# Kernel tuning notes

Measured on AMD Instinct MI355X. Metric: run time of the kernel, lower is better.

## Reference

```python
import jax, jax.numpy as jnp
import numpy as np

EPS_RMS = 1.1920929e-07  # torch F.rms_norm default eps = finfo(float32).eps
N_EMBD = 64
N_QKV = 256


def _silu(t):
    return t * jax.nn.sigmoid(t)


def _rms_norm(t):
    return t * jax.lax.rsqrt(jnp.mean(t * t, axis=-1, keepdims=True) + EPS_RMS)


def _w_norm(w, n):
    target_std = n ** (-0.5)
    return w * (target_std / (jnp.std(w, ddof=1) + 1e-08))


def setup_inputs() -> dict:
    key = jax.random.key(0)
    ks = jax.random.split(key, 7)
    B, T = 8, 8192
    x = jax.random.normal(ks[0], (B, T, N_EMBD), dtype=jnp.float32)
    y = jax.random.normal(ks[1], (B, T, N_QKV), dtype=jnp.float32)
    # CastedLinear init: uniform(-s, s), s = sqrt(3)/sqrt(in_features)
    def lin(k, out_f, in_f):
        s = (3.0 ** 0.5) * in_f ** (-0.5)
        return jax.random.uniform(k, (out_f, in_f), jnp.float32, -s, s)
    w_qkv = lin(ks[2], 3 * N_QKV, N_EMBD)          # [768, 64]
    w_swiglu = lin(ks[3], 2 * N_EMBD, N_QKV)       # [128, 256]
    w_out = lin(ks[4], N_EMBD, N_EMBD)             # [64, 64]
    out_w = lin(ks[5], N_EMBD, N_EMBD)             # self.out weight [64, 64]
    tao = lin(ks[6], 3, 1)                          # [3, 1]
    return {"x": x, "y": y, "w_qkv": w_qkv, "w_swiglu": w_swiglu,
            "w_out": w_out, "out_w": out_w, "tao": tao}


def reference(x, y, w_qkv, w_swiglu, w_out, out_w, tao):
    B = x.shape[0]
    # SwiGLU branch: F.linear(y, w_swiglu) -> [B,T,2*n_embd], chunk
    uv = jnp.einsum('btq,eq->bte', y, w_swiglu)
    u, v = jnp.split(uv, 2, axis=-1)                 # each [B,T,64]
    y_out = x + jnp.einsum('btd,ed->bte', u * _silu(v), w_out)

    # gates
    g = jnp.clip(jnp.abs(tao), 1e-08, 1.0)           # [3,1]
    alpha, beta, gamma = g[0], g[1], g[2]

    # Hebbian outer-product memory: mean_b(u^T v) * n_embd^-0.5, rms-normed
    ao = jnp.einsum('btd,bte->de', u, v) / B * (N_EMBD ** (-0.5))  # [64,64]
    ao = _rms_norm(ao)

    # update w_qkv
    n1 = _silu(w_qkv @ ao)                            # [768,64]
    w_qkv_new = _w_norm(w_qkv + n1 @ out_w.T, N_EMBD) * alpha

    # update w_swiglu: view(64, 512).T @ ao
    n2 = _silu(w_swiglu.reshape(N_EMBD, 2 * N_QKV).T @ ao)  # [512,64]
    n2 = n2 @ out_w.T                                  # [512,64]
    w_swiglu_new = w_swiglu + n2.T.reshape(2 * N_EMBD, N_QKV)
    w_swiglu_new = _w_norm(w_swiglu_new, N_QKV) * beta

    # update w_out
    n3 = _silu(w_out @ ao)                             # [64,64]
    w_out_new = _w_norm(w_out + n3 @ out_w.T, N_QKV) * gamma

    return (y_out, w_qkv_new, w_swiglu_new, w_out_new)
```

## Files before the change

### kernel.cpp

```cpp
#include <hip/hip_runtime.h>
#include <cstdint>

typedef short short8 __attribute__((ext_vector_type(8)));
typedef short short4_t __attribute__((ext_vector_type(4)));
typedef float floatx4 __attribute__((ext_vector_type(4)));

#define MFMA_BF16 __builtin_amdgcn_mfma_f32_16x16x32_bf16

__device__ __forceinline__ short f2bf(float f) {
  union { float f; unsigned u; } a; a.f = f;
  unsigned r = a.u + 0x7FFFu + ((a.u >> 16) & 1u);
  return (short)(r >> 16);
}
__device__ __forceinline__ float bf2f(short s) {
  union { unsigned u; float f; } a;
  a.u = ((unsigned)(unsigned short)s) << 16;
  return a.f;
}
__device__ __forceinline__ float silu_f(float v) {
  return v / (1.0f + __expf(-v));
}

#define QDIM 256
#define DEMB 64
#define TILE_T 32
#define ITERS 2
#define NBLK1 1024
#define YSTR 264
#define TSTR 40
#define HSTR 72

#define OFF_QKV 4194304
#define OFF_SW  4243456
#define OFF_WO  4276224

#define AO_COPIES 16
#define WS_SUMS   65536
#define WS_AOT    65544
#define WS_W1P    67592
#define WS_W2P    83976

__global__ __launch_bounds__(256) void k0_pack(
    const float* __restrict__ w_sw, const float* __restrict__ w_out,
    short* __restrict__ W1P, short* __restrict__ W2P,
    float* __restrict__ ws_base)
{
  int t = blockIdx.x * 256 + threadIdx.x;
  if (t < 16386) {
    float4 z = {0.f, 0.f, 0.f, 0.f};
    ((float4*)ws_base)[t] = z;
  }
  if (t < 4096) {
    int lane = t & 63, kt = (t >> 6) & 7, ntw = t >> 9;
    int row = (ntw >> 1) * 32 + (ntw & 1) * 16 + (lane & 15);
    int col = kt * 32 + (lane >> 4) * 8;
    const float* p = w_sw + row * QDIM + col;
    short8 f;
#pragma unroll
    for (int j = 0; j < 8; ++j) f[j] = f2bf(p[j]);
    ((short8*)W1P)[t] = f;
  } else if (t < 4608) {
    int u = t - 4096;
    int lane = u & 63, ktw = u >> 6;
    int row = (ktw >> 1) * 16 + (lane & 15);
    int col = (ktw & 1) * 32 + (lane >> 4) * 8;
    const float* p = w_out + row * DEMB + col;
    short8 f;
#pragma unroll
    for (int j = 0; j < 8; ++j) f[j] = f2bf(p[j]);
    ((short8*)W2P)[u] = f;
  }
}

__global__ __launch_bounds__(256, 3) void k1_main(
    const float* __restrict__ x, const float* __restrict__ y,
    const short* __restrict__ W1P, const short* __restrict__ W2P,
    float* __restrict__ y_out, float* __restrict__ ao_copies)
{
  __shared__ __align__(16) short Ylds[2][TILE_T * YSTR];
  __shared__ __align__(16) short UVT[128 * TSTR];
  __shared__ __align__(16) short Hlds[TILE_T * HSTR];

  const int tid  = threadIdx.x;
  const int lane = tid & 63;
  const int wave = tid >> 6;
  const int l15  = lane & 15;
  const int quad = lane >> 4;
  const floatx4 fzero = {0.f, 0.f, 0.f, 0.f};
  const int tok0 = blockIdx.x * (TILE_T * ITERS);

  const short8* W1v = (const short8*)W1P;
  const short8* W2v = (const short8*)W2P;
  short8 b1[2][8];
#pragma unroll
  for (int nt = 0; nt < 2; ++nt)
#pragma unroll
    for (int kt = 0; kt < 8; ++kt)
      b1[nt][kt] = W1v[((wave * 2 + nt) * 8 + kt) * 64 + lane];
  short8 b2[2];
#pragma unroll
  for (int kt = 0; kt < 2; ++kt)
    b2[kt] = W2v[(wave * 2 + kt) * 64 + lane];

  floatx4 ao_acc[4];
#pragma unroll
  for (int i = 0; i < 4; ++i) ao_acc[i] = fzero;

  float4 yreg[8];
  {
    const float4* src = (const float4*)(y + (size_t)tok0 * QDIM);
#pragma unroll
    for (int rep = 0; rep < 8; ++rep) yreg[rep] = src[tid + rep * 256];
#pragma unroll
    for (int rep = 0; rep < 8; ++rep) {
      int i = tid + rep * 256;
      int tok = i >> 6;
      int col = (i & 63) * 4;
      float4 f = yreg[rep];
      short4_t p4 = { f2bf(f.x), f2bf(f.y), f2bf(f.z), f2bf(f.w) };
      *(short4_t*)&Ylds[0][tok * YSTR + col] = p4;
    }
  }
  float xreg[8];
  __syncthreads();

  for (int it = 0; it < ITERS; ++it) {
    const int cur = it & 1;

    if (it + 1 < ITERS) {
      const float4* src = (const float4*)(y + (size_t)(tok0 + (it + 1) * TILE_T) * QDIM);
#pragma unroll
      for (int rep = 0; rep < 8; ++rep) yreg[rep] = src[tid + rep * 256];
    }
    if (it > 0) {
      const int tb = tok0 + (it - 1) * TILE_T;
#pragma unroll
      for (int mt = 0; mt < 2; ++mt) {
        floatx4 acc2 = fzero;
#pragma unroll
        for (int kt = 0; kt < 2; ++kt) {
          short8 a2 = *(const short8*)&Hlds[(mt * 16 + l15) * HSTR + kt * 32 + quad * 8];
          acc2 = MFMA_BF16(a2, b2[kt], acc2, 0, 0, 0);
        }
        int e = wave * 16 + l15;
#pragma unroll
        for (int r = 0; r < 4; ++r) {
          size_t idx = (size_t)(tb + mt * 16 + quad * 4 + r) * DEMB + e;
          y_out[idx] = xreg[mt * 4 + r] + acc2[r];
        }
      }
    }
    floatx4 acc[2][2];
#pragma unroll
    for (int a = 0; a < 2; ++a)
#pragma unroll
      for (int b = 0; b < 2; ++b) acc[a][b] = fzero;
#pragma unroll
    for (int kt = 0; kt < 8; ++kt) {
      short8 a0 = *(const short8*)&Ylds[cur][(l15)      * YSTR + kt * 32 + quad * 8];
      short8 a1 = *(const short8*)&Ylds[cur][(16 + l15) * YSTR + kt * 32 + quad * 8];
      acc[0][0] = MFMA_BF16(a0, b1[0][kt], acc[0][0], 0, 0, 0);
      acc[0][1] = MFMA_BF16(a0, b1[1][kt], acc[0][1], 0, 0, 0);
      acc[1][0] = MFMA_BF16(a1, b1[0][kt], acc[1][0], 0, 0, 0);
      acc[1][1] = MFMA_BF16(a1, b1[1][kt], acc[1][1], 0, 0, 0);
    }
#pragma unroll
    for (int mt = 0; mt < 2; ++mt)
#pragma unroll
      for (int nt = 0; nt < 2; ++nt) {
        short4_t p4;
#pragma unroll
        for (int r = 0; r < 4; ++r) p4[r] = f2bf(acc[mt][nt][r]);
        int c  = wave * 32 + nt * 16 + l15;
        int t0 = mt * 16 + quad * 4;
        *(short4_t*)&UVT[c * TSTR + t0] = p4;
      }
    __syncthreads();

    {
      const float* xb = x + (size_t)(tok0 + it * TILE_T) * DEMB + wave * 16 + l15;
#pragma unroll
      for (int mt = 0; mt < 2; ++mt)
#pragma unroll
        for (int r = 0; r < 4; ++r)
          xreg[mt * 4 + r] = xb[(mt * 16 + quad * 4 + r) * DEMB];
    }
    {
      int d  = tid & 63;
      int t0 = (tid >> 6) * 8;
      short8 u8 = *(const short8*)&UVT[d * TSTR + t0];
      short8 v8 = *(const short8*)&UVT[(64 + d) * TSTR + t0];
#pragma unroll
      for (int j = 0; j < 8; ++j) {
        float h = bf2f(u8[j]) * silu_f(bf2f(v8[j]));
        Hlds[(t0 + j) * HSTR + d] = f2bf(h);
      }
    }
    {
      short8 a3 = *(const short8*)&UVT[(wave * 16 + l15) * TSTR + quad * 8];
#pragma unroll
      for (int et = 0; et < 4; ++et) {
        short8 b3 = *(const short8*)&UVT[(64 + et * 16 + l15) * TSTR + quad * 8];
        ao_acc[et] = MFMA_BF16(a3, b3, ao_acc[et], 0, 0, 0);
      }
    }
    if (it + 1 < ITERS) {
#pragma unroll
      for (int rep = 0; rep < 8; ++rep) {
        int i = tid + rep * 256;
        int tok = i >> 6;
        int col = (i & 63) * 4;
        float4 f = yreg[rep];
        short4_t p4 = { f2bf(f.x), f2bf(f.y), f2bf(f.z), f2bf(f.w) };
        *(short4_t*)&Ylds[1 - cur][tok * YSTR + col] = p4;
      }
    }
    __syncthreads();
  }

  {
    const int tb = tok0 + (ITERS - 1) * TILE_T;
#pragma unroll
    for (int mt = 0; mt < 2; ++mt) {
      floatx4 acc2 = fzero;
#pragma unroll
      for (int kt = 0; kt < 2; ++kt) {
        short8 a2 = *(const short8*)&Hlds[(mt * 16 + l15) * HSTR + kt * 32 + quad * 8];
        acc2 = MFMA_BF16(a2, b2[kt], acc2, 0, 0, 0);
      }
      int e = wave * 16 + l15;
#pragma unroll
      for (int r = 0; r < 4; ++r) {
        size_t idx = (size_t)(tb + mt * 16 + quad * 4 + r) * DEMB + e;
        y_out[idx] = xreg[mt * 4 + r] + acc2[r];
      }
    }
  }

  float* dst = ao_copies + (blockIdx.x & (AO_COPIES - 1)) * 4096;
#pragma unroll
  for (int et = 0; et < 4; ++et)
#pragma unroll
    for (int r = 0; r < 4; ++r) {
      int d = wave * 16 + quad * 4 + r;
      int e = et * 16 + l15;
      atomicAdd(&dst[d * 64 + e], ao_acc[et][r]);
    }
}

__global__ __launch_bounds__(256) void k2_finalize(
    const float* __restrict__ ao_copies, unsigned short* __restrict__ aoT)
{
  __shared__ float aoFT[64 * 65];
  __shared__ float ssPart[256];
  __shared__ float scRow[64];
  const int tid = threadIdx.x;

#pragma unroll
  for (int k = 0; k < 16; ++k) {
    int idx = k * 256 + tid;
    float v = 0.f;
#pragma unroll
    for (int c = 0; c < AO_COPIES; ++c) v += ao_copies[c * 4096 + idx];
    v *= (1.0f / 64.0f);
    int d = idx >> 6, e = idx & 63;
    aoFT[e * 65 + d] = v;
  }
  __syncthreads();
  {
    int d = tid >> 2, q = tid & 3;
    float ssp = 0.f;
#pragma unroll
    for (int e2 = 0; e2 < 16; ++e2) {
      float v = aoFT[(q * 16 + e2) * 65 + d];
      ssp += v * v;
    }
    ssPart[tid] = ssp;
  }
  __syncthreads();
  if (tid < 64) {
    float ss = ssPart[tid * 4] + ssPart[tid * 4 + 1] +
               ssPart[tid * 4 + 2] + ssPart[tid * 4 + 3];
    scRow[tid] = rsqrtf(ss * (1.0f / 64.0f) + 1.1920929e-07f);
  }
  __syncthreads();
#pragma unroll
  for (int k = 0; k < 16; ++k) {
    int j = k * 256 + tid;
    int e = j >> 6, d = j & 63;
    aoT[j] = (unsigned short)f2bf(aoFT[e * 65 + d] * scRow[d]);
  }
}

__global__ __launch_bounds__(64) void k3_updates(
    const float* __restrict__ w_qkv, const float* __restrict__ w_sw,
    const float* __restrict__ w_out, const float* __restrict__ out_w,
    const unsigned short* __restrict__ aoT, float* __restrict__ out,
    float* __restrict__ sums)
{
  __shared__ __align__(16) short Nlds[16 * 72];
  const int lane = threadIdx.x;
  const int l15  = lane & 15;
  const int quad = lane >> 4;
  const int rid  = blockIdx.x;
  const floatx4 fzero = {0.f, 0.f, 0.f, 0.f};
  const short8* aoTv = (const short8*)aoT;

  short8 bf[2][4];
#pragma unroll
  for (int kt = 0; kt < 2; ++kt)
#pragma unroll
    for (int nt = 0; nt < 4; ++nt)
      bf[kt][nt] = aoTv[(nt * 16 + l15) * 8 + kt * 4 + quad];

  short8 af[2];
  if (rid < 48) {
    const float* wr = w_qkv + (size_t)(rid * 16 + l15) * 64;
#pragma unroll
    for (int kt = 0; kt < 2; ++kt) {
      const float* p = wr + kt * 32 + quad * 8;
      short8 f;
#pragma unroll
      for (int j = 0; j < 8; ++j) f[j] = f2bf(p[j]);
      af[kt] = f;
    }
  } else if (rid < 80) {
    int p0 = (rid - 48) * 16;
#pragma unroll
    for (int kt = 0; kt < 2; ++kt) {
      short8 f;
#pragma unroll
      for (int j = 0; j < 8; ++j) {
        int a = kt * 32 + quad * 8 + j;
        f[j] = f2bf(w_sw[a * 512 + p0 + l15]);
      }
      af[kt] = f;
    }
  } else {
    const float* wr = w_out + (size_t)((rid - 80) * 16 + l15) * 64;
#pragma unroll
    for (int kt = 0; kt < 2; ++kt) {
      const float* p = wr + kt * 32 + quad * 8;
      short8 f;
#pragma unroll
      for (int j = 0; j < 8; ++j) f[j] = f2bf(p[j]);
      af[kt] = f;
    }
  }

  floatx4 acc[4];
#pragma unroll
  for (int nt = 0; nt < 4; ++nt) acc[nt] = fzero;
#pragma unroll
  for (int kt = 0; kt < 2; ++kt)
#pragma unroll
    for (int nt = 0; nt < 4; ++nt)
      acc[nt] = MFMA_BF16(af[kt], bf[kt][nt], acc[nt], 0, 0, 0);
#pragma unroll
  for (int nt = 0; nt < 4; ++nt)
#pragma unroll
    for (int r = 0; r < 4; ++r)
      Nlds[(quad * 4 + r) * 72 + nt * 16 + l15] = f2bf(silu_f(acc[nt][r]));
  __syncthreads();

  float s1 = 0.f, s2 = 0.f;
  int matrix;

  if (rid < 48 || rid >= 80) {
    matrix = (rid < 48) ? 0 : 2;
    short8 a2[2];
#pragma unroll
    for (int kt = 0; kt < 2; ++kt)
      a2[kt] = *(const short8*)&Nlds[l15 * 72 + kt * 32 + quad * 8];
    short8 b2[2][4];
#pragma unroll
    for (int nt = 0; nt < 4; ++nt) {
      const float* wr = out_w + (size_t)(nt * 16 + l15) * 64;
#pragma unroll
      for (int kt = 0; kt < 2; ++kt) {
        const float* p = wr + kt * 32 + quad * 8;
        short8 f;
#pragma unroll
        for (int j = 0; j < 8; ++j) f[j] = f2bf(p[j]);
        b2[kt][nt] = f;
      }
    }
    floatx4 acc2[4];
#pragma unroll
    for (int nt = 0; nt < 4; ++nt) acc2[nt] = fzero;
#pragma unroll
    for (int kt = 0; kt < 2; ++kt)
#pragma unroll
      for (int nt = 0; nt < 4; ++nt)
        acc2[nt] = MFMA_BF16(a2[kt], b2[kt][nt], acc2[nt], 0, 0, 0);

    const float* Wsrc = (rid < 48) ? w_qkv : w_out;
    int base_row = (rid < 48) ? rid * 16 : (rid - 80) * 16;
    int off      = (rid < 48) ? OFF_QKV : OFF_WO;
#pragma unroll
    for (int nt = 0; nt < 4; ++nt)
#pragma unroll
      for (int r = 0; r < 4; ++r) {
        int row = base_row + quad * 4 + r;
        int col = nt * 16 + l15;
        float val = Wsrc[row * 64 + col] + acc2[nt][r];
        out[off + row * 64 + col] = val;
        s1 += val; s2 += val * val;
      }
  } else {
    matrix = 1;
    int p0 = (rid - 48) * 16;
    short8 b2[2];
#pragma unroll
    for (int kt = 0; kt < 2; ++kt)
      b2[kt] = *(const short8*)&Nlds[l15 * 72 + kt * 32 + quad * 8];
    short8 a2[4][2];
#pragma unroll
    for (int mt = 0; mt < 4; ++mt) {
      const float* wr = out_w + (size_t)(mt * 16 + l15) * 64;
#pragma unroll
      for (int kt = 0; kt < 2; ++kt) {
        const float* p = wr + kt * 32 + quad * 8;
        short8 f;
#pragma unroll
        for (int j = 0; j < 8; ++j) f[j] = f2bf(p[j]);
        a2[mt][kt] = f;
      }
    }
    floatx4 acc2[4];
#pragma unroll
    for (int mt = 0; mt < 4; ++mt) acc2[mt] = fzero;
#pragma unroll
    for (int mt = 0; mt < 4; ++mt)
#pragma unroll
      for (int kt = 0; kt < 2; ++kt)
        acc2[mt] = MFMA_BF16(a2[mt][kt], b2[kt], acc2[mt], 0, 0, 0);
#pragma unroll
    for (int mt = 0; mt < 4; ++mt)
#pragma unroll
      for (int r = 0; r < 4; ++r) {
        int a = mt * 16 + quad * 4 + r;
        int p = p0 + l15;
        int idx = a * 512 + p;
        float val = w_sw[idx] + acc2[mt][r];
        out[OFF_SW + idx] = val;
        s1 += val; s2 += val * val;
      }
  }

#pragma unroll
  for (int off = 32; off > 0; off >>= 1) {
    s1 += __shfl_down(s1, off);
    s2 += __shfl_down(s2, off);
  }
  if (lane == 0) {
    atomicAdd(&sums[matrix * 2],     s1);
    atomicAdd(&sums[matrix * 2 + 1], s2);
  }
}

__global__ __launch_bounds__(256) void k4_scale(
    float* __restrict__ out, const float* __restrict__ sums,
    const float* __restrict__ tao)
{
  int i = blockIdx.x * 256 + threadIdx.x;
  int matrix, idx; float N, tstd;
  if (i < 49152)      { matrix = 0; idx = OFF_QKV + i;           N = 49152.f; tstd = 0.125f;  }
  else if (i < 81920) { matrix = 1; idx = OFF_SW + (i - 49152);  N = 32768.f; tstd = 0.0625f; }
  else                { matrix = 2; idx = OFF_WO + (i - 81920);  N = 4096.f;  tstd = 0.0625f; }
  float sum = sums[matrix * 2], sumsq = sums[matrix * 2 + 1];
  float mean = sum / N;
  float var  = (sumsq - N * mean * mean) / (N - 1.f);
  float sd   = sqrtf(fmaxf(var, 0.f));
  float g    = fminf(fmaxf(fabsf(tao[matrix]), 1e-8f), 1.0f);
  out[idx] *= g * tstd / (sd + 1e-8f);
}

extern "C" void kernel_launch(void* const* d_in, const int* in_sizes, int n_in,
                              void* d_out, int out_size, void* d_ws, size_t ws_size,
                              hipStream_t stream) {
  const float* x     = (const float*)d_in[0];
  const float* y     = (const float*)d_in[1];
  const float* w_qkv = (const float*)d_in[2];
  const float* w_sw  = (const float*)d_in[3];
  const float* w_out = (const float*)d_in[4];
  const float* out_w = (const float*)d_in[5];
  const float* tao   = (const float*)d_in[6];
  float* out = (float*)d_out;
  float* ws  = (float*)d_ws;

  float* ao_copies    = ws;
  float* sums         = ws + WS_SUMS;
  unsigned short* aoT = (unsigned short*)(ws + WS_AOT);
  short* W1P          = (short*)(ws + WS_W1P);
  short* W2P          = (short*)(ws + WS_W2P);

  k0_pack<<<dim3(65), dim3(256), 0, stream>>>(w_sw, w_out, W1P, W2P, ws);
  k1_main<<<dim3(NBLK1), dim3(256), 0, stream>>>(x, y, W1P, W2P, out, ao_copies);
  k2_finalize<<<dim3(1), dim3(256), 0, stream>>>(ao_copies, aoT);
  k3_updates<<<dim3(84), dim3(64), 0, stream>>>(w_qkv, w_sw, w_out, out_w,
                                                aoT, out, sums);
  k4_scale<<<dim3(336), dim3(256), 0, stream>>>(out, sums, tao);
}
```

Before: 143.1 us.

## Fuse ao finalize into update kernel; use nontemporal loads/stores in main kernel

Merges the single-block ao finalize kernel into the weight-update kernel. Each of 21 four-wave blocks now redundantly reduces the ao copies, RMS-normalises them and keeps the transposed bf16 ao in LDS, which removes one launch and a global round trip. The main kernel also switches the streaming x/y loads and y_out stores to nontemporal builtins, and silu uses a fast divide. The cost is that every update block repeats the 16-copy reduction.

```diff
diff --git a/kernel.cpp b/kernel.cpp
--- a/kernel.cpp
+++ b/kernel.cpp
@@ -4,6 +4,7 @@
 typedef short short8 __attribute__((ext_vector_type(8)));
 typedef short short4_t __attribute__((ext_vector_type(4)));
 typedef float floatx4 __attribute__((ext_vector_type(4)));
+typedef float floatv4 __attribute__((ext_vector_type(4)));
 
 #define MFMA_BF16 __builtin_amdgcn_mfma_f32_16x16x32_bf16
 
@@ -18,7 +19,7 @@
   return a.f;
 }
 __device__ __forceinline__ float silu_f(float v) {
-  return v / (1.0f + __expf(-v));
+  return v * __fdividef(1.0f, 1.0f + __expf(-v));
 }
 
 #define QDIM 256
@@ -36,9 +37,8 @@
 
 #define AO_COPIES 16
 #define WS_SUMS   65536
-#define WS_AOT    65544
-#define WS_W1P    67592
-#define WS_W2P    83976
+#define WS_W1P    65544
+#define WS_W2P    81928
 
 __global__ __launch_bounds__(256) void k0_pack(
     const float* __restrict__ w_sw, const float* __restrict__ w_out,
@@ -106,17 +106,18 @@
 #pragma unroll
   for (int i = 0; i < 4; ++i) ao_acc[i] = fzero;
 
-  float4 yreg[8];
+  floatv4 yreg[8];
   {
-    const float4* src = (const float4*)(y + (size_t)tok0 * QDIM);
-#pragma unroll
-    for (int rep = 0; rep < 8; ++rep) yreg[rep] = src[tid + rep * 256];
+    const floatv4* src = (const floatv4*)(y + (size_t)tok0 * QDIM);
+#pragma unroll
+    for (int rep = 0; rep < 8; ++rep)
+      yreg[rep] = __builtin_nontemporal_load(&src[tid + rep * 256]);
 #pragma unroll
     for (int rep = 0; rep < 8; ++rep) {
       int i = tid + rep * 256;
       int tok = i >> 6;
       int col = (i & 63) * 4;
-      float4 f = yreg[rep];
+      floatv4 f = yreg[rep];
       short4_t p4 = { f2bf(f.x), f2bf(f.y), f2bf(f.z), f2bf(f.w) };
       *(short4_t*)&Ylds[0][tok * YSTR + col] = p4;
     }
@@ -128,9 +129,10 @@
     const int cur = it & 1;
 
     if (it + 1 < ITERS) {
-      const float4* src = (const float4*)(y + (size_t)(tok0 + (it + 1) * TILE_T) * QDIM);
-#pragma unroll
-      for (int rep = 0; rep < 8; ++rep) yreg[rep] = src[tid + rep * 256];
+      const floatv4* src = (const floatv4*)(y + (size_t)(tok0 + (it + 1) * TILE_T) * QDIM);
+#pragma unroll
+      for (int rep = 0; rep < 8; ++rep)
+        yreg[rep] = __builtin_nontemporal_load(&src[tid + rep * 256]);
     }
     if (it > 0) {
       const int tb = tok0 + (it - 1) * TILE_T;
@@ -146,7 +148,7 @@
 #pragma unroll
         for (int r = 0; r < 4; ++r) {
           size_t idx = (size_t)(tb + mt * 16 + quad * 4 + r) * DEMB + e;
-          y_out[idx] = xreg[mt * 4 + r] + acc2[r];
+          __builtin_nontemporal_store(xreg[mt * 4 + r] + acc2[r], &y_out[idx]);
         }
       }
     }
@@ -183,7 +185,7 @@
       for (int mt = 0; mt < 2; ++mt)
 #pragma unroll
         for (int r = 0; r < 4; ++r)
-          xreg[mt * 4 + r] = xb[(mt * 16 + quad * 4 + r) * DEMB];
+          xreg[mt * 4 + r] = __builtin_nontemporal_load(&xb[(mt * 16 + quad * 4 + r) * DEMB]);
     }
     {
       int d  = tid & 63;
@@ -210,7 +212,7 @@
         int i = tid + rep * 256;
         int tok = i >> 6;
         int col = (i & 63) * 4;
-        float4 f = yreg[rep];
+        floatv4 f = yreg[rep];
         short4_t p4 = { f2bf(f.x), f2bf(f.y), f2bf(f.z), f2bf(f.w) };
         *(short4_t*)&Ylds[1 - cur][tok * YSTR + col] = p4;
       }
@@ -232,7 +234,7 @@
 #pragma unroll
       for (int r = 0; r < 4; ++r) {
         size_t idx = (size_t)(tb + mt * 16 + quad * 4 + r) * DEMB + e;
-        y_out[idx] = xreg[mt * 4 + r] + acc2[r];
+        __builtin_nontemporal_store(xreg[mt * 4 + r] + acc2[r], &y_out[idx]);
       }
     }
   }
@@ -248,13 +250,24 @@
     }
 }
 
-__global__ __launch_bounds__(256) void k2_finalize(
-    const float* __restrict__ ao_copies, unsigned short* __restrict__ aoT)
+__global__ __launch_bounds__(256) void k3_updates(
+    const float* __restrict__ w_qkv, const float* __restrict__ w_sw,
+    const float* __restrict__ w_out, const float* __restrict__ out_w,
+    const float* __restrict__ ao_copies, float* __restrict__ out,
+    float* __restrict__ sums)
 {
   __shared__ float aoFT[64 * 65];
   __shared__ float ssPart[256];
   __shared__ float scRow[64];
-  const int tid = threadIdx.x;
+  __shared__ __align__(16) short aoT[64 * 72];
+  __shared__ __align__(16) short Nlds[4][16 * 72];
+
+  const int tid  = threadIdx.x;
+  const int lane = tid & 63;
+  const int wave = tid >> 6;
+  const int l15  = lane & 15;
+  const int quad = lane >> 4;
+  const floatx4 fzero = {0.f, 0.f, 0.f, 0.f};
 
 #pragma unroll
   for (int k = 0; k < 16; ++k) {
@@ -288,30 +301,18 @@
   for (int k = 0; k < 16; ++k) {
     int j = k * 256 + tid;
     int e = j >> 6, d = j & 63;
-    aoT[j] = (unsigned short)f2bf(aoFT[e * 65 + d] * scRow[d]);
-  }
-}
-
-__global__ __launch_bounds__(64) void k3_updates(
-    const float* __restrict__ w_qkv, const float* __restrict__ w_sw,
-    const float* __restrict__ w_out, const float* __restrict__ out_w,
-    const unsigned short* __restrict__ aoT, float* __restrict__ out,
-    float* __restrict__ sums)
-{
-  __shared__ __align__(16) short Nlds[16 * 72];
-  const int lane = threadIdx.x;
-  const int l15  = lane & 15;
-  const int quad = lane >> 4;
-  const int rid  = blockIdx.x;
-  const floatx4 fzero = {0.f, 0.f, 0.f, 0.f};
-  const short8* aoTv = (const short8*)aoT;
+    aoT[e * 72 + d] = f2bf(aoFT[e * 65 + d] * scRow[d]);
+  }
+  __syncthreads();
+
+  const int rid = blockIdx.x * 4 + wave;
 
   short8 bf[2][4];
 #pragma unroll
   for (int kt = 0; kt < 2; ++kt)
 #pragma unroll
     for (int nt = 0; nt < 4; ++nt)
-      bf[kt][nt] = aoTv[(nt * 16 + l15) * 8 + kt * 4 + quad];
+      bf[kt][nt] = *(const short8*)&aoT[(nt * 16 + l15) * 72 + kt * 32 + quad * 8];
 
   short8 af[2];
   if (rid < 48) {
@@ -360,7 +361,7 @@
   for (int nt = 0; nt < 4; ++nt)
 #pragma unroll
     for (int r = 0; r < 4; ++r)
-      Nlds[(quad * 4 + r) * 72 + nt * 16 + l15] = f2bf(silu_f(acc[nt][r]));
+      Nlds[wave][(quad * 4 + r) * 72 + nt * 16 + l15] = f2bf(silu_f(acc[nt][r]));
   __syncthreads();
 
   float s1 = 0.f, s2 = 0.f;
@@ -371,7 +372,7 @@
     short8 a2[2];
 #pragma unroll
     for (int kt = 0; kt < 2; ++kt)
-      a2[kt] = *(const short8*)&Nlds[l15 * 72 + kt * 32 + quad * 8];
+      a2[kt] = *(const short8*)&Nlds[wave][l15 * 72 + kt * 32 + quad * 8];
     short8 b2[2][4];
 #pragma unroll
     for (int nt = 0; nt < 4; ++nt) {
@@ -413,7 +414,7 @@
     short8 b2[2];
 #pragma unroll
     for (int kt = 0; kt < 2; ++kt)
-      b2[kt] = *(const short8*)&Nlds[l15 * 72 + kt * 32 + quad * 8];
+      b2[kt] = *(const short8*)&Nlds[wave][l15 * 72 + kt * 32 + quad * 8];
     short8 a2[4][2];
 #pragma unroll
     for (int mt = 0; mt < 4; ++mt) {
@@ -489,16 +490,14 @@
   float* out = (float*)d_out;
   float* ws  = (float*)d_ws;
 
-  float* ao_copies    = ws;
-  float* sums         = ws + WS_SUMS;
-  unsigned short* aoT = (unsigned short*)(ws + WS_AOT);
-  short* W1P          = (short*)(ws + WS_W1P);
-  short* W2P          = (short*)(ws + WS_W2P);
+  float* ao_copies = ws;
+  float* sums      = ws + WS_SUMS;
+  short* W1P       = (short*)(ws + WS_W1P);
+  short* W2P       = (short*)(ws + WS_W2P);
 
   k0_pack<<<dim3(65), dim3(256), 0, stream>>>(w_sw, w_out, W1P, W2P, ws);
   k1_main<<<dim3(NBLK1), dim3(256), 0, stream>>>(x, y, W1P, W2P, out, ao_copies);
-  k2_finalize<<<dim3(1), dim3(256), 0, stream>>>(ao_copies, aoT);
-  k3_updates<<<dim3(84), dim3(64), 0, stream>>>(w_qkv, w_sw, w_out, out_w,
-                                                aoT, out, sums);
+  k3_updates<<<dim3(21), dim3(256), 0, stream>>>(w_qkv, w_sw, w_out, out_w,
+                                                 ao_copies, out, sums);
   k4_scale<<<dim3(336), dim3(256), 0, stream>>>(out, sums, tao);
 }
```

Result: slower. 189.9 us (+32.7%).
